# Optimization experiments

Hardware: AMD Instinct MI355X
Metric: run time of the kernel (lower is better)

Reference implementation:

```python
import jax, jax.numpy as jnp
import numpy as np

NEG_SLOPE = 0.2  # PyG GATConv default negative_slope


def gat_conv(x, W, a_src, a_dst, bias, src, dst, heads, out_c, concat):
    """PyG-style GATConv with self-loops. x:[N,F_in], W:[F_in,heads*out_c]."""
    N = x.shape[0]
    # add self loops
    loop = jnp.arange(N, dtype=src.dtype)
    src = jnp.concatenate([src, loop])
    dst = jnp.concatenate([dst, loop])
    h = (x @ W).reshape(N, heads, out_c)            # [N,H,C]
    alpha_src = jnp.sum(h * a_src, axis=-1)          # [N,H]
    alpha_dst = jnp.sum(h * a_dst, axis=-1)          # [N,H]
    e = jax.nn.leaky_relu(alpha_src[src] + alpha_dst[dst], NEG_SLOPE)  # [E,H]
    # segment softmax over incoming edges of each destination node
    m = jax.ops.segment_max(e, dst, num_segments=N)  # [N,H]
    ex = jnp.exp(e - m[dst])
    s = jax.ops.segment_sum(ex, dst, num_segments=N)
    alpha = ex / (s[dst] + 1e-16)                    # [E,H]
    msg = h[src] * alpha[:, :, None]                 # [E,H,C]
    out = jax.ops.segment_sum(msg, dst, num_segments=N)  # [N,H,C]
    out = out.reshape(N, heads * out_c) if concat else out.mean(axis=1)
    return out + bias


def setup_inputs() -> dict:
    key = jax.random.key(0)
    ks = jax.random.split(key, 16)
    N, E = 25000, 400000
    node_dim, hidden, out_dim, heads = 64, 128, 256, 4

    def glorot(k, shape):
        fan = shape[0] + shape[-1]
        return jax.random.normal(k, shape, jnp.float32) * np.sqrt(2.0 / fan)

    return {
        "x": jax.random.normal(ks[0], (N, node_dim), jnp.float32),
        "edge_index": jax.random.randint(ks[1], (2, E), 0, N, jnp.int32),
        "W_emb": glorot(ks[2], (node_dim, hidden)),
        "b_emb": jnp.zeros((hidden,), jnp.float32),
        "W1": glorot(ks[3], (hidden, heads * hidden)),
        "a1_src": glorot(ks[4], (heads, hidden)),
        "a1_dst": glorot(ks[5], (heads, hidden)),
        "b1": jnp.zeros((heads * hidden,), jnp.float32),
        "W2": glorot(ks[6], (heads * hidden, hidden)),
        "a2_src": glorot(ks[7], (1, hidden)),
        "a2_dst": glorot(ks[8], (1, hidden)),
        "b2": jnp.zeros((hidden,), jnp.float32),
        "W_out": glorot(ks[9], (hidden, out_dim)),
        "b_out": jnp.zeros((out_dim,), jnp.float32),
    }


def reference(x, edge_index, W_emb, b_emb, W1, a1_src, a1_dst, b1, W2, a2_src, a2_dst, b2, W_out, b_out):
    src, dst = edge_index[0], edge_index[1]
    heads, hidden = a1_src.shape[0], a1_src.shape[1]
    h = jax.nn.relu(x @ W_emb + b_emb)                 # dropout is identity in eval
    h = gat_conv(h, W1, a1_src, a1_dst, b1, src, dst, heads, hidden, True)
    h = jax.nn.elu(h)
    h = gat_conv(h, W2, a2_src, a2_dst, b2, src, dst, 1, hidden, False)
    h = jax.nn.elu(h)
    g = jnp.mean(h, axis=0, keepdims=True)             # global mean pool, batch=None -> [1, hidden]
    return g @ W_out + b_out                           # [1, out_dim]
```

## Files before the change

### kernel.cpp

```cpp
#include <hip/hip_runtime.h>
#include <hip/hip_bf16.h>


#define LRELU(x) ((x) > 0.f ? (x) : 0.2f * (x))

typedef short bf16x8 __attribute__((ext_vector_type(8)));
typedef float f32x4 __attribute__((ext_vector_type(4)));
typedef float f32x2 __attribute__((ext_vector_type(2)));

static __device__ __forceinline__ unsigned short f2b(float f) {
    union { float f; unsigned u; } x; x.f = f;
    unsigned r = x.u + 0x7fff + ((x.u >> 16) & 1);
    return (unsigned short)(r >> 16);
}
static __device__ __forceinline__ float rl_f(float v, int c) {
    return __int_as_float(__builtin_amdgcn_readlane(__float_as_int(v), c));
}
static __device__ __forceinline__ unsigned char f2fp8(float v) {
    int p = __builtin_amdgcn_cvt_pk_fp8_f32(v, v, 0, false);
    return (unsigned char)(p & 0xff);
}

__global__ void zero_kernel(int* __restrict__ deg, int* __restrict__ cursor,
                            float* __restrict__ pool, int* __restrict__ done, int N) {
    int i = blockIdx.x * blockDim.x + threadIdx.x;
    if (i < N) deg[i] = 0;
    else if (i < 2 * N) cursor[i - N] = 0;
    else if (i < 2 * N + 128) pool[i - 2 * N] = 0.f;
    else if (i == 2 * N + 128) *done = 0;
}

__global__ void deg_count_kernel(const int* __restrict__ ei, int E, int N, int* __restrict__ deg) {
    int i = blockIdx.x * blockDim.x + threadIdx.x;
    if (i < E) atomicAdd(&deg[ei[E + i]], 1);
    else if (i < E + N) atomicAdd(&deg[i - E], 1);
}

__global__ __launch_bounds__(256) void scan_pass1(const int* __restrict__ deg, int* __restrict__ rowptr,
                                                  int* __restrict__ bsum, int N) {
    __shared__ int sd[256];
    int t = threadIdx.x, i = blockIdx.x * 256 + t;
    int d = (i < N) ? deg[i] : 0;
    sd[t] = d;
    __syncthreads();
    for (int off = 1; off < 256; off <<= 1) {
        int v = (t >= off) ? sd[t - off] : 0;
        __syncthreads();
        sd[t] += v;
        __syncthreads();
    }
    if (i < N) rowptr[i] = sd[t] - d;
    if (t == 255) bsum[blockIdx.x] = sd[t];
}

__global__ __launch_bounds__(128) void scan_pass2(const int* __restrict__ bsum, int* __restrict__ boff,
                                                  int* __restrict__ rowptr, int nb, int N) {
    __shared__ int sd[128];
    int t = threadIdx.x;
    int d = (t < nb) ? bsum[t] : 0;
    sd[t] = d;
    __syncthreads();
    for (int off = 1; off < 128; off <<= 1) {
        int v = (t >= off) ? sd[t - off] : 0;
        __syncthreads();
        sd[t] += v;
        __syncthreads();
    }
    if (t < nb) boff[t] = sd[t] - d;
    if (t == 127) rowptr[N] = sd[t];
}

__global__ __launch_bounds__(256) void scan_pass3(int* __restrict__ rowptr, const int* __restrict__ boff, int N) {
    int i = blockIdx.x * 256 + threadIdx.x;
    if (i < N) rowptr[i] += boff[blockIdx.x];
}

__global__ void scatter_kernel(const int* __restrict__ ei, int E, int N,
                               const int* __restrict__ rowptr, int* __restrict__ cursor,
                               int* __restrict__ esrc) {
    int i = blockIdx.x * blockDim.x + threadIdx.x;
    int s, d;
    if (i < E) { s = ei[i]; d = ei[E + i]; }
    else if (i < E + N) { s = i - E; d = s; }
    else return;
    int pos = rowptr[d] + atomicAdd(&cursor[d], 1);
    esrc[pos] = s;
}

__global__ void prep_kernel(const float* __restrict__ x, const float* __restrict__ We,
                            const float* __restrict__ W1, const float* __restrict__ W2,
                            unsigned short* __restrict__ xb, unsigned short* __restrict__ WeT,
                            unsigned short* __restrict__ W1T, unsigned short* __restrict__ W2T,
                            int Nx) {
    int i = blockIdx.x * blockDim.x + threadIdx.x;
    if (i < Nx) { xb[i] = f2b(x[i]); return; }
    i -= Nx;
    if (i < 64 * 128) { int k = i >> 7, n = i & 127; WeT[n * 64 + k] = f2b(We[i]); return; }
    i -= 64 * 128;
    if (i < 128 * 512) { int k = i >> 9, n = i & 511; W1T[n * 128 + k] = f2b(W1[i]); return; }
    i -= 128 * 512;
    if (i < 512 * 128) { int k = i >> 7, n = i & 127; W2T[n * 512 + k] = f2b(W2[i]); return; }
}

__global__ __launch_bounds__(256) void gemm12_fused(const unsigned short* __restrict__ A,
                                                    const unsigned short* __restrict__ WeT,
                                                    const float* __restrict__ b_emb,
                                                    const unsigned short* __restrict__ W1T,
                                                    unsigned char* __restrict__ C8,
                                                    const float* __restrict__ a_src,
                                                    const float* __restrict__ a_dst,
                                                    float* __restrict__ as_out,
                                                    float* __restrict__ ad_out, int M) {
    __shared__ __align__(16) unsigned short smem[22016];
    unsigned short* Asx = smem;
    unsigned short* Bwe = smem + 9216;
    unsigned short* h0s = smem;
    unsigned short* Bs  = smem + 16896;
    __shared__ float sAl[128][2];

    int tid = threadIdx.x;
    int gm0 = blockIdx.y * 128, gn0 = blockIdx.x * 128;
    int w = tid >> 6, lane = tid & 63;
    int wrow = (w >> 1) * 64, wcol = (w & 1) * 64;
    int l15 = lane & 15, quad = lane >> 4;

    f32x4 acc[4][4];
#pragma unroll
    for (int i = 0; i < 4; i++)
#pragma unroll
        for (int j = 0; j < 4; j++) acc[i][j] = {0.f, 0.f, 0.f, 0.f};

#pragma unroll
    for (int rr = 0; rr < 4; rr++) {
        int lin = tid + rr * 256;
        int row = lin >> 3;
        int cg = (lin & 7) * 8;
        int grow = gm0 + row; if (grow >= M) grow = M - 1;
        *(uint4*)&Asx[row * 72 + cg] = *(const uint4*)&A[(size_t)grow * 64 + cg];
        *(uint4*)&Bwe[row * 72 + cg] = *(const uint4*)&WeT[(size_t)row * 64 + cg];
    }
    __syncthreads();
#pragma unroll
    for (int k0 = 0; k0 < 64; k0 += 32) {
        bf16x8 af[4], bfr[4];
#pragma unroll
        for (int i = 0; i < 4; i++) {
            af[i]  = *(const bf16x8*)&Asx[(wrow + i * 16 + l15) * 72 + k0 + quad * 8];
            bfr[i] = *(const bf16x8*)&Bwe[(wcol + i * 16 + l15) * 72 + k0 + quad * 8];
        }
#pragma unroll
        for (int i = 0; i < 4; i++)
#pragma unroll
            for (int j = 0; j < 4; j++)
                acc[i][j] = __builtin_amdgcn_mfma_f32_16x16x32_bf16(af[i], bfr[j], acc[i][j], 0, 0, 0);
    }
    __syncthreads();

#pragma unroll
    for (int j = 0; j < 4; j++) {
        int col = wcol + j * 16 + l15;
        float bv = b_emb[col];
#pragma unroll
        for (int i = 0; i < 4; i++) {
            int row = wrow + i * 16 + quad * 4;
#pragma unroll
            for (int r = 0; r < 4; r++) {
                float v = fmaxf(acc[i][j][r] + bv, 0.f);
                h0s[(row + r) * 132 + col] = f2b(v);
            }
        }
    }

#pragma unroll
    for (int i = 0; i < 4; i++)
#pragma unroll
        for (int j = 0; j < 4; j++) acc[i][j] = {0.f, 0.f, 0.f, 0.f};

    for (int k0 = 0; k0 < 128; k0 += 32) {
#pragma unroll
        for (int rr = 0; rr < 2; rr++) {
            int lin = tid + rr * 256;
            int row = lin >> 2;
            int cg = (lin & 3) * 8;
            *(uint4*)&Bs[row * 40 + cg] = *(const uint4*)&W1T[(size_t)(gn0 + row) * 128 + k0 + cg];
        }
        __syncthreads();
        bf16x8 af[4], bfr[4];
#pragma unroll
        for (int i = 0; i < 4; i++) {
            af[i]  = *(const bf16x8*)&h0s[(wrow + i * 16 + l15) * 132 + k0 + quad * 8];
            bfr[i] = *(const bf16x8*)&Bs[(wcol + i * 16 + l15) * 40 + quad * 8];
        }
#pragma unroll
        for (int i = 0; i < 4; i++)
#pragma unroll
            for (int j = 0; j < 4; j++)
                acc[i][j] = __builtin_amdgcn_mfma_f32_16x16x32_bf16(af[i], bfr[j], acc[i][j], 0, 0, 0);
        __syncthreads();
    }

#pragma unroll
    for (int i = 0; i < 4; i++) {
        int row = gm0 + wrow + i * 16 + quad * 4;
#pragma unroll
        for (int j = 0; j < 4; j++) {
            int col = gn0 + wcol + j * 16 + l15;
#pragma unroll
            for (int r = 0; r < 4; r++) {
                int gr = row + r;
                if (gr < M) C8[(size_t)gr * 512 + col] = f2fp8(acc[i][j][r]);
            }
        }
    }

    {
        int hh = blockIdx.x;
        float as_c[4], ad_c[4];
#pragma unroll
        for (int j = 0; j < 4; j++) {
            int c = gn0 + wcol + j * 16 + l15;
            as_c[j] = a_src[c];
            ad_c[j] = a_dst[c];
        }
#pragma unroll
        for (int i = 0; i < 4; i++) {
#pragma unroll
            for (int r = 0; r < 4; r++) {
                float ps = 0.f, pd = 0.f;
#pragma unroll
                for (int j = 0; j < 4; j++) {
                    ps += acc[i][j][r] * as_c[j];
                    pd += acc[i][j][r] * ad_c[j];
                }
#pragma unroll
                for (int o = 1; o < 16; o <<= 1) {
                    ps += __shfl_xor(ps, o);
                    pd += __shfl_xor(pd, o);
                }
                if (wcol == 64 && l15 == 0) {
                    int lr = wrow + i * 16 + quad * 4 + r;
                    sAl[lr][0] = ps;
                    sAl[lr][1] = pd;
                }
            }
        }
        __syncthreads();
        if (wcol == 0) {
#pragma unroll
            for (int i = 0; i < 4; i++) {
#pragma unroll
                for (int r = 0; r < 4; r++) {
                    float ps = 0.f, pd = 0.f;
#pragma unroll
                    for (int j = 0; j < 4; j++) {
                        ps += acc[i][j][r] * as_c[j];
                        pd += acc[i][j][r] * ad_c[j];
                    }
#pragma unroll
                    for (int o = 1; o < 16; o <<= 1) {
                        ps += __shfl_xor(ps, o);
                        pd += __shfl_xor(pd, o);
                    }
                    if (l15 == 0) {
                        int lr = wrow + i * 16 + quad * 4 + r;
                        int gr = gm0 + lr;
                        if (gr < M) {
                            as_out[(size_t)gr * 4 + hh] = ps + sAl[lr][0];
                            ad_out[(size_t)gr * 4 + hh] = pd + sAl[lr][1];
                        }
                    }
                }
            }
        }
    }
}

template <int ACT, int OFMT, int ALPHA, int H>
__global__ __launch_bounds__(256) void gemm_mfma_nt(const unsigned short* __restrict__ A,
                                                    const unsigned short* __restrict__ Bt,
                                                    const float* __restrict__ bias,
                                                    void* __restrict__ Cout,
                                                    const float* __restrict__ a_src,
                                                    const float* __restrict__ a_dst,
                                                    float* __restrict__ as_out,
                                                    float* __restrict__ ad_out,
                                                    int M, int N, int K) {
    __shared__ __align__(16) unsigned short As[128 * 40];
    __shared__ __align__(16) unsigned short Bs[128 * 40];
    __shared__ float sAl[128][2];
    int tid = threadIdx.x;
    int gm0 = blockIdx.y * 128, gn0 = blockIdx.x * 128;
    int w = tid >> 6, lane = tid & 63;
    int wrow = (w >> 1) * 64, wcol = (w & 1) * 64;
    int l15 = lane & 15, quad = lane >> 4;

    f32x4 acc[4][4];
#pragma unroll
    for (int i = 0; i < 4; i++)
#pragma unroll
        for (int j = 0; j < 4; j++) acc[i][j] = {0.f, 0.f, 0.f, 0.f};

    for (int k0 = 0; k0 < K; k0 += 32) {
#pragma unroll
        for (int rr = 0; rr < 2; rr++) {
            int lin = tid + rr * 256;
            int row = lin >> 2;
            int cg = (lin & 3) * 8;
            int grow = gm0 + row; if (grow >= M) grow = M - 1;
            uint4 va = *(const uint4*)&A[(size_t)grow * K + k0 + cg];
            *(uint4*)&As[row * 40 + cg] = va;
            uint4 vb = *(const uint4*)&Bt[(size_t)(gn0 + row) * K + k0 + cg];
            *(uint4*)&Bs[row * 40 + cg] = vb;
        }
        __syncthreads();
        bf16x8 af[4], bfr[4];
#pragma unroll
        for (int i = 0; i < 4; i++) {
            af[i]  = *(const bf16x8*)&As[(wrow + i * 16 + l15) * 40 + quad * 8];
            bfr[i] = *(const bf16x8*)&Bs[(wcol + i * 16 + l15) * 40 + quad * 8];
        }
#pragma unroll
        for (int i = 0; i < 4; i++)
#pragma unroll
            for (int j = 0; j < 4; j++)
                acc[i][j] = __builtin_amdgcn_mfma_f32_16x16x32_bf16(af[i], bfr[j], acc[i][j], 0, 0, 0);
        __syncthreads();
    }

    if (OFMT == 0) {
        unsigned short* C = (unsigned short*)Cout;
#pragma unroll
        for (int i = 0; i < 4; i++) {
            int row = gm0 + wrow + i * 16 + quad * 4;
#pragma unroll
            for (int j = 0; j < 4; j++) {
                int col = gn0 + wcol + j * 16 + l15;
                float bv = bias ? bias[col] : 0.f;
#pragma unroll
                for (int r = 0; r < 4; r++) {
                    int gr = row + r;
                    if (gr < M) {
                        float v = acc[i][j][r] + bv;
                        if (ACT == 1) v = fmaxf(v, 0.f);
                        C[(size_t)gr * N + col] = f2b(v);
                    }
                }
            }
        }
    } else {
        unsigned char* C8 = (unsigned char*)Cout;
#pragma unroll
        for (int i = 0; i < 4; i++) {
            int row = gm0 + wrow + i * 16 + quad * 4;
#pragma unroll
            for (int j = 0; j < 4; j++) {
                int col = gn0 + wcol + j * 16 + l15;
#pragma unroll
                for (int r = 0; r < 4; r++) {
                    int gr = row + r;
                    if (gr < M) C8[(size_t)gr * N + col] = f2fp8(acc[i][j][r]);
                }
            }
        }
    }

    if (ALPHA) {
        int hh = blockIdx.x;
        float as_c[4], ad_c[4];
#pragma unroll
        for (int j = 0; j < 4; j++) {
            int c = gn0 + wcol + j * 16 + l15;
            as_c[j] = a_src[c];
            ad_c[j] = a_dst[c];
        }
#pragma unroll
        for (int i = 0; i < 4; i++) {
#pragma unroll
            for (int r = 0; r < 4; r++) {
                float ps = 0.f, pd = 0.f;
#pragma unroll
                for (int j = 0; j < 4; j++) {
                    ps += acc[i][j][r] * as_c[j];
                    pd += acc[i][j][r] * ad_c[j];
                }
#pragma unroll
                for (int o = 1; o < 16; o <<= 1) {
                    ps += __shfl_xor(ps, o);
                    pd += __shfl_xor(pd, o);
                }
                if (wcol == 64 && l15 == 0) {
                    int lr = wrow + i * 16 + quad * 4 + r;
                    sAl[lr][0] = ps;
                    sAl[lr][1] = pd;
                }
            }
        }
        __syncthreads();
        if (wcol == 0) {
#pragma unroll
            for (int i = 0; i < 4; i++) {
#pragma unroll
                for (int r = 0; r < 4; r++) {
                    float ps = 0.f, pd = 0.f;
#pragma unroll
                    for (int j = 0; j < 4; j++) {
                        ps += acc[i][j][r] * as_c[j];
                        pd += acc[i][j][r] * ad_c[j];
                    }
#pragma unroll
                    for (int o = 1; o < 16; o <<= 1) {
                        ps += __shfl_xor(ps, o);
                        pd += __shfl_xor(pd, o);
                    }
                    if (l15 == 0) {
                        int lr = wrow + i * 16 + quad * 4 + r;
                        int gr = gm0 + lr;
                        if (gr < M) {
                            as_out[(size_t)gr * H + hh] = ps + sAl[lr][0];
                            ad_out[(size_t)gr * H + hh] = pd + sAl[lr][1];
                        }
                    }
                }
            }
        }
    }
}

__global__ __launch_bounds__(256) void gat_agg_l1(const unsigned* __restrict__ hq,
                                                  const float4* __restrict__ as4,
                                                  const float4* __restrict__ ad4,
                                                  const int* __restrict__ rowptr,
                                                  const int* __restrict__ esrc,
                                                  const float* __restrict__ bias,
                                                  unsigned short* __restrict__ out, int N) {
    __shared__ float wlds_all[4][256];
    int w = threadIdx.x >> 6, lane = threadIdx.x & 63;
    int n = blockIdx.x * 4 + w;
    if (n >= N) return;
    float* wlds = wlds_all[w];
    int begin = rowptr[n], deg = rowptr[n + 1] - begin;
    float4 adn = ad4[n];

    int s_l0 = 0;
    float4 e0 = {-3.4e38f, -3.4e38f, -3.4e38f, -3.4e38f};
    if (lane < deg) {
        s_l0 = esrc[begin + lane];
        float4 u = as4[s_l0];
        e0.x = LRELU(u.x + adn.x); e0.y = LRELU(u.y + adn.y);
        e0.z = LRELU(u.z + adn.z); e0.w = LRELU(u.w + adn.w);
    }
    float4 m = e0;
    for (int base = 64; base < deg; base += 64) {
        int j = base + lane;
        if (j < deg) {
            float4 u = as4[esrc[begin + j]];
            m.x = fmaxf(m.x, LRELU(u.x + adn.x)); m.y = fmaxf(m.y, LRELU(u.y + adn.y));
            m.z = fmaxf(m.z, LRELU(u.z + adn.z)); m.w = fmaxf(m.w, LRELU(u.w + adn.w));
        }
    }
#pragma unroll
    for (int o = 32; o >= 1; o >>= 1) {
        m.x = fmaxf(m.x, __shfl_xor(m.x, o));
        m.y = fmaxf(m.y, __shfl_xor(m.y, o));
        m.z = fmaxf(m.z, __shfl_xor(m.z, o));
        m.w = fmaxf(m.w, __shfl_xor(m.w, o));
    }
    float4 s4 = {0.f, 0.f, 0.f, 0.f};
    if (lane < deg) {
        s4.x = __expf(e0.x - m.x); s4.y = __expf(e0.y - m.y);
        s4.z = __expf(e0.z - m.z); s4.w = __expf(e0.w - m.w);
    }
    for (int base = 64; base < deg; base += 64) {
        int j = base + lane;
        if (j < deg) {
            float4 u = as4[esrc[begin + j]];
            s4.x += __expf(LRELU(u.x + adn.x) - m.x); s4.y += __expf(LRELU(u.y + adn.y) - m.y);
            s4.z += __expf(LRELU(u.z + adn.z) - m.z); s4.w += __expf(LRELU(u.w + adn.w) - m.w);
        }
    }
#pragma unroll
    for (int o = 32; o >= 1; o >>= 1) {
        s4.x += __shfl_xor(s4.x, o); s4.y += __shfl_xor(s4.y, o);
        s4.z += __shfl_xor(s4.z, o); s4.w += __shfl_xor(s4.w, o);
    }
    float4 inv = {1.f / (s4.x + 1e-16f), 1.f / (s4.y + 1e-16f),
                  1.f / (s4.z + 1e-16f), 1.f / (s4.w + 1e-16f)};

    float acc[8] = {};
    int h = lane >> 4;
#define ACC_E1(q, wgt) { \
    f32x2 p0 = __builtin_amdgcn_cvt_pk_f32_fp8((int)q.x, false); \
    f32x2 p1 = __builtin_amdgcn_cvt_pk_f32_fp8((int)q.x, true);  \
    f32x2 p2 = __builtin_amdgcn_cvt_pk_f32_fp8((int)q.y, false); \
    f32x2 p3 = __builtin_amdgcn_cvt_pk_f32_fp8((int)q.y, true);  \
    acc[0] += wgt * p0.x; acc[1] += wgt * p0.y; acc[2] += wgt * p1.x; acc[3] += wgt * p1.y; \
    acc[4] += wgt * p2.x; acc[5] += wgt * p2.y; acc[6] += wgt * p3.x; acc[7] += wgt * p3.y; }

    for (int base = 0; base < deg; base += 64) {
        int j = base + lane;
        int len = min(64, deg - base);
        int s_l = s_l0;
        float4 e = e0;
        if (base > 0 && j < deg) {
            s_l = esrc[begin + j];
            float4 u = as4[s_l];
            e.x = LRELU(u.x + adn.x); e.y = LRELU(u.y + adn.y);
            e.z = LRELU(u.z + adn.z); e.w = LRELU(u.w + adn.w);
        }
        if (j < deg) {
            float4 wv4 = {__expf(e.x - m.x) * inv.x, __expf(e.y - m.y) * inv.y,
                          __expf(e.z - m.z) * inv.z, __expf(e.w - m.w) * inv.w};
            *(float4*)&wlds[lane * 4] = wv4;
        }
        int c = 0;
        for (; c + 4 <= len; c += 4) {
            int s0 = __builtin_amdgcn_readlane(s_l, c);
            int s1 = __builtin_amdgcn_readlane(s_l, c + 1);
            int s2 = __builtin_amdgcn_readlane(s_l, c + 2);
            int s3 = __builtin_amdgcn_readlane(s_l, c + 3);
            uint2 q0 = *((const uint2*)(hq + (size_t)s0 * 128) + lane);
            uint2 q1 = *((const uint2*)(hq + (size_t)s1 * 128) + lane);
            uint2 q2 = *((const uint2*)(hq + (size_t)s2 * 128) + lane);
            uint2 q3 = *((const uint2*)(hq + (size_t)s3 * 128) + lane);
            float w0 = wlds[c * 4 + h];
            float w1 = wlds[c * 4 + 4 + h];
            float w2 = wlds[c * 4 + 8 + h];
            float w3 = wlds[c * 4 + 12 + h];
            ACC_E1(q0, w0); ACC_E1(q1, w1); ACC_E1(q2, w2); ACC_E1(q3, w3);
        }
        for (; c < len; c++) {
            int s0 = __builtin_amdgcn_readlane(s_l, c);
            uint2 q0 = *((const uint2*)(hq + (size_t)s0 * 128) + lane);
            float w0 = wlds[c * 4 + h];
            ACC_E1(q0, w0);
        }
    }
#undef ACC_E1
    int f0 = lane * 8;
    unsigned pk[4];
#pragma unroll
    for (int k = 0; k < 4; k++) {
        float v0 = acc[2 * k] + bias[f0 + 2 * k];
        float v1 = acc[2 * k + 1] + bias[f0 + 2 * k + 1];
        v0 = v0 > 0.f ? v0 : (__expf(v0) - 1.f);
        v1 = v1 > 0.f ? v1 : (__expf(v1) - 1.f);
        pk[k] = (unsigned)f2b(v0) | ((unsigned)f2b(v1) << 16);
    }
    uint4 pv = {pk[0], pk[1], pk[2], pk[3]};
    *((uint4*)(out + (size_t)n * 512) + lane) = pv;
}

__global__ __launch_bounds__(256) void gat_agg_l2(const unsigned char* __restrict__ hq,
                                                  const float* __restrict__ as,
                                                  const float* __restrict__ ad,
                                                  const int* __restrict__ rowptr,
                                                  const int* __restrict__ esrc,
                                                  const float* __restrict__ bias,
                                                  float* __restrict__ out, int N) {
    int w = threadIdx.x >> 6, lane = threadIdx.x & 63;
    int n = blockIdx.x * 4 + w;
    if (n >= N) return;
    int begin = rowptr[n], deg = rowptr[n + 1] - begin;
    float adn = ad[n];

    int s_l0 = 0;
    float e0 = -3.4e38f;
    if (lane < deg) {
        s_l0 = esrc[begin + lane];
        e0 = LRELU(as[s_l0] + adn);
    }
    float m = e0;
    for (int base = 64; base < deg; base += 64) {
        int j = base + lane;
        if (j < deg) m = fmaxf(m, LRELU(as[esrc[begin + j]] + adn));
    }
#pragma unroll
    for (int o = 32; o >= 1; o >>= 1) m = fmaxf(m, __shfl_xor(m, o));

    float s = (lane < deg) ? __expf(e0 - m) : 0.f;
    for (int base = 64; base < deg; base += 64) {
        int j = base + lane;
        if (j < deg) s += __expf(LRELU(as[esrc[begin + j]] + adn) - m);
    }
#pragma unroll
    for (int o = 32; o >= 1; o >>= 1) s += __shfl_xor(s, o);
    float inv = 1.f / (s + 1e-16f);

    float acc0 = 0.f, acc1 = 0.f;
    for (int base = 0; base < deg; base += 64) {
        int j = base + lane;
        int len = min(64, deg - base);
        int s_l = s_l0;
        float e = e0;
        if (base > 0 && j < deg) {
            s_l = esrc[begin + j];
            e = LRELU(as[s_l] + adn);
        }
        float w_l = (j < deg) ? __expf(e - m) * inv : 0.f;
        int c = 0;
        for (; c + 4 <= len; c += 4) {
            int sp0 = __builtin_amdgcn_readlane(s_l, c);
            int sp1 = __builtin_amdgcn_readlane(s_l, c + 1);
            int sp2 = __builtin_amdgcn_readlane(s_l, c + 2);
            int sp3 = __builtin_amdgcn_readlane(s_l, c + 3);
            unsigned short u0 = *((const unsigned short*)(hq + (size_t)sp0 * 128) + lane);
            unsigned short u1 = *((const unsigned short*)(hq + (size_t)sp1 * 128) + lane);
            unsigned short u2 = *((const unsigned short*)(hq + (size_t)sp2 * 128) + lane);
            unsigned short u3 = *((const unsigned short*)(hq + (size_t)sp3 * 128) + lane);
            float w0 = rl_f(w_l, c), w1 = rl_f(w_l, c + 1);
            float w2 = rl_f(w_l, c + 2), w3 = rl_f(w_l, c + 3);
            f32x2 p0 = __builtin_amdgcn_cvt_pk_f32_fp8((int)u0, false);
            f32x2 p1 = __builtin_amdgcn_cvt_pk_f32_fp8((int)u1, false);
            f32x2 p2 = __builtin_amdgcn_cvt_pk_f32_fp8((int)u2, false);
            f32x2 p3 = __builtin_amdgcn_cvt_pk_f32_fp8((int)u3, false);
            acc0 += w0 * p0.x; acc1 += w0 * p0.y;
            acc0 += w1 * p1.x; acc1 += w1 * p1.y;
            acc0 += w2 * p2.x; acc1 += w2 * p2.y;
            acc0 += w3 * p3.x; acc1 += w3 * p3.y;
        }
        for (; c < len; c++) {
            int sp0 = __builtin_amdgcn_readlane(s_l, c);
            float w0 = rl_f(w_l, c);
            unsigned short u0 = *((const unsigned short*)(hq + (size_t)sp0 * 128) + lane);
            f32x2 p0 = __builtin_amdgcn_cvt_pk_f32_fp8((int)u0, false);
            acc0 += w0 * p0.x; acc1 += w0 * p0.y;
        }
    }
    float v0 = acc0 + bias[lane * 2];
    float v1 = acc1 + bias[lane * 2 + 1];
    v0 = v0 > 0.f ? v0 : (__expf(v0) - 1.f);
    v1 = v1 > 0.f ? v1 : (__expf(v1) - 1.f);
    float2 pv = {v0, v1};
    *(float2*)&out[(size_t)n * 128 + lane * 2] = pv;
}

__global__ __launch_bounds__(256) void pool_final_kernel(const float* __restrict__ o2,
                                                         float* __restrict__ pool,
                                                         int* __restrict__ done,
                                                         const float* __restrict__ Wout,
                                                         const float* __restrict__ bout,
                                                         float* __restrict__ out,
                                                         int N, int nblocks, float invN) {
    __shared__ float4 sred[256];
    int f4 = threadIdx.x & 31;
    int r = blockIdx.x * 256 + (threadIdx.x >> 5);
    float4 acc = {0.f, 0.f, 0.f, 0.f};
    for (int i = 0; i < 32; i++, r += 8) {
        if (r < N) {
            float4 v = *(const float4*)&o2[(size_t)r * 128 + f4 * 4];
            acc.x += v.x; acc.y += v.y; acc.z += v.z; acc.w += v.w;
        }
    }
    sred[threadIdx.x] = acc;
    __syncthreads();
    if (threadIdx.x < 32) {
        float4 t = sred[threadIdx.x];
#pragma unroll
        for (int k = 1; k < 8; k++) {
            float4 u = sred[threadIdx.x + 32 * k];
            t.x += u.x; t.y += u.y; t.z += u.z; t.w += u.w;
        }
        atomicAdd(&pool[f4 * 4 + 0], t.x);
        atomicAdd(&pool[f4 * 4 + 1], t.y);
        atomicAdd(&pool[f4 * 4 + 2], t.z);
        atomicAdd(&pool[f4 * 4 + 3], t.w);
    }
    __threadfence();
    __shared__ int isLast;
    if (threadIdx.x == 0) isLast = (atomicAdd(done, 1) == nblocks - 1);
    __syncthreads();
    if (isLast) {
        __shared__ float spool[128];
        if (threadIdx.x < 128) spool[threadIdx.x] = atomicAdd(&pool[threadIdx.x], 0.f);
        __syncthreads();
        int o = threadIdx.x;
        float a = 0.f;
        for (int k = 0; k < 128; k++) a += spool[k] * Wout[k * 256 + o];
        out[o] = a * invN + bout[o];
    }
}

extern "C" void kernel_launch(void* const* d_in, const int* in_sizes, int n_in,
                              void* d_out, int out_size, void* d_ws, size_t ws_size,
                              hipStream_t stream) {
    const float* x      = (const float*)d_in[0];
    const int*   ei     = (const int*)d_in[1];
    const float* W_emb  = (const float*)d_in[2];
    const float* b_emb  = (const float*)d_in[3];
    const float* W1     = (const float*)d_in[4];
    const float* a1_src = (const float*)d_in[5];
    const float* a1_dst = (const float*)d_in[6];
    const float* b1     = (const float*)d_in[7];
    const float* W2     = (const float*)d_in[8];
    const float* a2_src = (const float*)d_in[9];
    const float* a2_dst = (const float*)d_in[10];
    const float* b2     = (const float*)d_in[11];
    const float* W_out  = (const float*)d_in[12];
    const float* b_out  = (const float*)d_in[13];
    float* out = (float*)d_out;

    const int N = in_sizes[0] / 64;
    const int E = in_sizes[1] / 2;
    const int Etot = E + N;
    const int nb = (N + 255) / 256;

    char* ws = (char*)d_ws;
    size_t off = 0;
    auto alloc = [&](size_t bytes) -> void* {
        void* p = ws + off;
        off = (off + bytes + 255) & ~(size_t)255;
        return p;
    };
    typedef unsigned short u16;
    u16* xb    = (u16*)alloc((size_t)N * 64 * 2);
    u16* WeT   = (u16*)alloc((size_t)128 * 64 * 2);
    u16* W1T   = (u16*)alloc((size_t)512 * 128 * 2);
    u16* W2T   = (u16*)alloc((size_t)128 * 512 * 2);
    unsigned char* h1q = (unsigned char*)alloc((size_t)N * 512);
    u16* o1b   = (u16*)alloc((size_t)N * 512 * 2);
    unsigned char* h2q = (unsigned char*)alloc((size_t)N * 128);
    float* o2  = (float*)alloc((size_t)N * 128 * 4);
    float* as1 = (float*)alloc((size_t)N * 4 * 4);
    float* ad1 = (float*)alloc((size_t)N * 4 * 4);
    float* as2 = (float*)alloc((size_t)N * 4);
    float* ad2 = (float*)alloc((size_t)N * 4);
    float* pool = (float*)alloc(128 * 4);
    int* done   = (int*)alloc(256);
    int* rowptr = (int*)alloc((size_t)(N + 1) * 4);
    int* deg    = (int*)alloc((size_t)N * 4);
    int* cursor = (int*)alloc((size_t)N * 4);
    int* bsum   = (int*)alloc(128 * 4);
    int* boff   = (int*)alloc(128 * 4);
    int* esrc   = (int*)alloc((size_t)Etot * 4);

    zero_kernel<<<(2 * N + 129 + 255) / 256, 256, 0, stream>>>(deg, cursor, pool, done, N);
    int blocksE = (Etot + 255) / 256;
    deg_count_kernel<<<blocksE, 256, 0, stream>>>(ei, E, N, deg);
    scan_pass1<<<nb, 256, 0, stream>>>(deg, rowptr, bsum, N);
    scan_pass2<<<1, 128, 0, stream>>>(bsum, boff, rowptr, nb, N);
    scan_pass3<<<nb, 256, 0, stream>>>(rowptr, boff, N);
    scatter_kernel<<<blocksE, 256, 0, stream>>>(ei, E, N, rowptr, cursor, esrc);

    int Nx = N * 64;
    int prep_elems = Nx + 64 * 128 + 128 * 512 + 512 * 128;
    prep_kernel<<<(prep_elems + 255) / 256, 256, 0, stream>>>(x, W_emb, W1, W2, xb, WeT, W1T, W2T, Nx);

    int mtiles = (N + 127) / 128;
    gemm12_fused<<<dim3(4, mtiles), 256, 0, stream>>>(xb, WeT, b_emb, W1T, h1q,
                                                      a1_src, a1_dst, as1, ad1, N);

    gat_agg_l1<<<(N + 3) / 4, 256, 0, stream>>>((const unsigned*)h1q, (const float4*)as1,
                                                (const float4*)ad1, rowptr, esrc, b1, o1b, N);

    gemm_mfma_nt<0, 1, 1, 1><<<dim3(1, mtiles), 256, 0, stream>>>(
        o1b, W2T, nullptr, h2q, a2_src, a2_dst, as2, ad2, N, 128, 512);

    gat_agg_l2<<<(N + 3) / 4, 256, 0, stream>>>(h2q, as2, ad2, rowptr, esrc, b2, o2, N);

    int npb = (N + 255) / 256;
    pool_final_kernel<<<npb, 256, 0, stream>>>(o2, pool, done, W_out, b_out, out,
                                               N, npb, 1.f / (float)N);
}
```

Before: 277.3 us.

## Fuse prep into degree count, drop scan pass3, unroll gather loops by 8

Merges the bf16 conversion and weight-transpose prep kernel into the degree-count kernel. It removes the third scan pass by adding per-block offsets (boff) at every rowptr read in scatter and both aggregation kernels. The gather loops in both GAT aggregation kernels go from 4 to 8 loads in flight. This cuts two kernel launches and increases memory-level parallelism, at the cost of extra boff lookups and higher register pressure.

```diff
diff --git a/kernel.cpp b/kernel.cpp
--- a/kernel.cpp
+++ b/kernel.cpp
@@ -30,10 +30,25 @@
     else if (i == 2 * N + 128) *done = 0;
 }
 
-__global__ void deg_count_kernel(const int* __restrict__ ei, int E, int N, int* __restrict__ deg) {
+__global__ void prep_count_kernel(const int* __restrict__ ei, int E, int N,
+                                  int* __restrict__ deg,
+                                  const float* __restrict__ x, const float* __restrict__ We,
+                                  const float* __restrict__ W1, const float* __restrict__ W2,
+                                  unsigned short* __restrict__ xb, unsigned short* __restrict__ WeT,
+                                  unsigned short* __restrict__ W1T, unsigned short* __restrict__ W2T,
+                                  int Nx) {
     int i = blockIdx.x * blockDim.x + threadIdx.x;
-    if (i < E) atomicAdd(&deg[ei[E + i]], 1);
-    else if (i < E + N) atomicAdd(&deg[i - E], 1);
+    if (i < E) { atomicAdd(&deg[ei[E + i]], 1); return; }
+    i -= E;
+    if (i < N) { atomicAdd(&deg[i], 1); return; }
+    i -= N;
+    if (i < Nx) { xb[i] = f2b(x[i]); return; }
+    i -= Nx;
+    if (i < 64 * 128) { int k = i >> 7, n = i & 127; WeT[n * 64 + k] = f2b(We[i]); return; }
+    i -= 64 * 128;
+    if (i < 128 * 512) { int k = i >> 9, n = i & 511; W1T[n * 128 + k] = f2b(W1[i]); return; }
+    i -= 128 * 512;
+    if (i < 512 * 128) { int k = i >> 7, n = i & 127; W2T[n * 512 + k] = f2b(W2[i]); return; }
 }
 
 __global__ __launch_bounds__(256) void scan_pass1(const int* __restrict__ deg, int* __restrict__ rowptr,
@@ -49,12 +64,12 @@
         sd[t] += v;
         __syncthreads();
     }
-    if (i < N) rowptr[i] = sd[t] - d;
+    if (i <= N) rowptr[i] = sd[t] - d;
     if (t == 255) bsum[blockIdx.x] = sd[t];
 }
 
 __global__ __launch_bounds__(128) void scan_pass2(const int* __restrict__ bsum, int* __restrict__ boff,
-                                                  int* __restrict__ rowptr, int nb, int N) {
+                                                  int nb) {
     __shared__ int sd[128];
     int t = threadIdx.x;
     int d = (t < nb) ? bsum[t] : 0;
@@ -67,39 +82,18 @@
         __syncthreads();
     }
     if (t < nb) boff[t] = sd[t] - d;
-    if (t == 127) rowptr[N] = sd[t];
-}
-
-__global__ __launch_bounds__(256) void scan_pass3(int* __restrict__ rowptr, const int* __restrict__ boff, int N) {
-    int i = blockIdx.x * 256 + threadIdx.x;
-    if (i < N) rowptr[i] += boff[blockIdx.x];
 }
 
 __global__ void scatter_kernel(const int* __restrict__ ei, int E, int N,
-                               const int* __restrict__ rowptr, int* __restrict__ cursor,
-                               int* __restrict__ esrc) {
+                               const int* __restrict__ rowptr, const int* __restrict__ boff,
+                               int* __restrict__ cursor, int* __restrict__ esrc) {
     int i = blockIdx.x * blockDim.x + threadIdx.x;
     int s, d;
     if (i < E) { s = ei[i]; d = ei[E + i]; }
     else if (i < E + N) { s = i - E; d = s; }
     else return;
-    int pos = rowptr[d] + atomicAdd(&cursor[d], 1);
+    int pos = rowptr[d] + boff[d >> 8] + atomicAdd(&cursor[d], 1);
     esrc[pos] = s;
-}
-
-__global__ void prep_kernel(const float* __restrict__ x, const float* __restrict__ We,
-                            const float* __restrict__ W1, const float* __restrict__ W2,
-                            unsigned short* __restrict__ xb, unsigned short* __restrict__ WeT,
-                            unsigned short* __restrict__ W1T, unsigned short* __restrict__ W2T,
-                            int Nx) {
-    int i = blockIdx.x * blockDim.x + threadIdx.x;
-    if (i < Nx) { xb[i] = f2b(x[i]); return; }
-    i -= Nx;
-    if (i < 64 * 128) { int k = i >> 7, n = i & 127; WeT[n * 64 + k] = f2b(We[i]); return; }
-    i -= 64 * 128;
-    if (i < 128 * 512) { int k = i >> 9, n = i & 511; W1T[n * 128 + k] = f2b(W1[i]); return; }
-    i -= 128 * 512;
-    if (i < 512 * 128) { int k = i >> 7, n = i & 127; W2T[n * 512 + k] = f2b(W2[i]); return; }
 }
 
 __global__ __launch_bounds__(256) void gemm12_fused(const unsigned short* __restrict__ A,
@@ -430,6 +424,7 @@
                                                   const float4* __restrict__ as4,
                                                   const float4* __restrict__ ad4,
                                                   const int* __restrict__ rowptr,
+                                                  const int* __restrict__ boff,
                                                   const int* __restrict__ esrc,
                                                   const float* __restrict__ bias,
                                                   unsigned short* __restrict__ out, int N) {
@@ -438,7 +433,8 @@
     int n = blockIdx.x * 4 + w;
     if (n >= N) return;
     float* wlds = wlds_all[w];
-    int begin = rowptr[n], deg = rowptr[n + 1] - begin;
+    int begin = rowptr[n] + boff[n >> 8];
+    int deg = rowptr[n + 1] + boff[(n + 1) >> 8] - begin;
     float4 adn = ad4[n];
 
     int s_l0 = 0;
@@ -513,24 +509,22 @@
             *(float4*)&wlds[lane * 4] = wv4;
         }
         int c = 0;
-        for (; c + 4 <= len; c += 4) {
-            int s0 = __builtin_amdgcn_readlane(s_l, c);
-            int s1 = __builtin_amdgcn_readlane(s_l, c + 1);
-            int s2 = __builtin_amdgcn_readlane(s_l, c + 2);
-            int s3 = __builtin_amdgcn_readlane(s_l, c + 3);
-            uint2 q0 = *((const uint2*)(hq + (size_t)s0 * 128) + lane);
-            uint2 q1 = *((const uint2*)(hq + (size_t)s1 * 128) + lane);
-            uint2 q2 = *((const uint2*)(hq + (size_t)s2 * 128) + lane);
-            uint2 q3 = *((const uint2*)(hq + (size_t)s3 * 128) + lane);
-            float w0 = wlds[c * 4 + h];
-            float w1 = wlds[c * 4 + 4 + h];
-            float w2 = wlds[c * 4 + 8 + h];
-            float w3 = wlds[c * 4 + 12 + h];
-            ACC_E1(q0, w0); ACC_E1(q1, w1); ACC_E1(q2, w2); ACC_E1(q3, w3);
+        for (; c + 8 <= len; c += 8) {
+            uint2 q[8];
+#pragma unroll
+            for (int t = 0; t < 8; t++) {
+                int sp = __builtin_amdgcn_readlane(s_l, c + t);
+                q[t] = *((const uint2*)(hq + (size_t)sp * 128) + lane);
+            }
+#pragma unroll
+            for (int t = 0; t < 8; t++) {
+                float wt = wlds[(c + t) * 4 + h];
+                ACC_E1(q[t], wt);
+            }
         }
         for (; c < len; c++) {
-            int s0 = __builtin_amdgcn_readlane(s_l, c);
-            uint2 q0 = *((const uint2*)(hq + (size_t)s0 * 128) + lane);
+            int sp = __builtin_amdgcn_readlane(s_l, c);
+            uint2 q0 = *((const uint2*)(hq + (size_t)sp * 128) + lane);
             float w0 = wlds[c * 4 + h];
             ACC_E1(q0, w0);
         }
@@ -554,13 +548,15 @@
                                                   const float* __restrict__ as,
                                                   const float* __restrict__ ad,
                                                   const int* __restrict__ rowptr,
+                                                  const int* __restrict__ boff,
                                                   const int* __restrict__ esrc,
                                                   const float* __restrict__ bias,
                                                   float* __restrict__ out, int N) {
     int w = threadIdx.x >> 6, lane = threadIdx.x & 63;
     int n = blockIdx.x * 4 + w;
     if (n >= N) return;
-    int begin = rowptr[n], deg = rowptr[n + 1] - begin;
+    int begin = rowptr[n] + boff[n >> 8];
+    int deg = rowptr[n + 1] + boff[(n + 1) >> 8] - begin;
     float adn = ad[n];
 
     int s_l0 = 0;
@@ -598,30 +594,25 @@
         }
         float w_l = (j < deg) ? __expf(e - m) * inv : 0.f;
         int c = 0;
-        for (; c + 4 <= len; c += 4) {
-            int sp0 = __builtin_amdgcn_readlane(s_l, c);
-            int sp1 = __builtin_amdgcn_readlane(s_l, c + 1);
-            int sp2 = __builtin_amdgcn_readlane(s_l, c + 2);
-            int sp3 = __builtin_amdgcn_readlane(s_l, c + 3);
-            unsigned short u0 = *((const unsigned short*)(hq + (size_t)sp0 * 128) + lane);
-            unsigned short u1 = *((const unsigned short*)(hq + (size_t)sp1 * 128) + lane);
-            unsigned short u2 = *((const unsigned short*)(hq + (size_t)sp2 * 128) + lane);
-            unsigned short u3 = *((const unsigned short*)(hq + (size_t)sp3 * 128) + lane);
-            float w0 = rl_f(w_l, c), w1 = rl_f(w_l, c + 1);
-            float w2 = rl_f(w_l, c + 2), w3 = rl_f(w_l, c + 3);
-            f32x2 p0 = __builtin_amdgcn_cvt_pk_f32_fp8((int)u0, false);
-            f32x2 p1 = __builtin_amdgcn_cvt_pk_f32_fp8((int)u1, false);
-            f32x2 p2 = __builtin_amdgcn_cvt_pk_f32_fp8((int)u2, false);
-            f32x2 p3 = __builtin_amdgcn_cvt_pk_f32_fp8((int)u3, false);
-            acc0 += w0 * p0.x; acc1 += w0 * p0.y;
-            acc0 += w1 * p1.x; acc1 += w1 * p1.y;
-            acc0 += w2 * p2.x; acc1 += w2 * p2.y;
-            acc0 += w3 * p3.x; acc1 += w3 * p3.y;
+        for (; c + 8 <= len; c += 8) {
+            unsigned short u[8];
+            float wt[8];
+#pragma unroll
+            for (int t = 0; t < 8; t++) {
+                int sp = __builtin_amdgcn_readlane(s_l, c + t);
+                u[t] = *((const unsigned short*)(hq + (size_t)sp * 128) + lane);
+                wt[t] = rl_f(w_l, c + t);
+            }
+#pragma unroll
+            for (int t = 0; t < 8; t++) {
+                f32x2 p = __builtin_amdgcn_cvt_pk_f32_fp8((int)u[t], false);
+                acc0 += wt[t] * p.x; acc1 += wt[t] * p.y;
+            }
         }
         for (; c < len; c++) {
-            int sp0 = __builtin_amdgcn_readlane(s_l, c);
+            int sp = __builtin_amdgcn_readlane(s_l, c);
             float w0 = rl_f(w_l, c);
-            unsigned short u0 = *((const unsigned short*)(hq + (size_t)sp0 * 128) + lane);
+            unsigned short u0 = *((const unsigned short*)(hq + (size_t)sp * 128) + lane);
             f32x2 p0 = __builtin_amdgcn_cvt_pk_f32_fp8((int)u0, false);
             acc0 += w0 * p0.x; acc1 += w0 * p0.y;
         }
@@ -702,7 +693,7 @@
     const int N = in_sizes[0] / 64;
     const int E = in_sizes[1] / 2;
     const int Etot = E + N;
-    const int nb = (N + 255) / 256;
+    const int nb = (N + 256) / 256;
 
     char* ws = (char*)d_ws;
     size_t off = 0;
@@ -734,29 +725,23 @@
     int* esrc   = (int*)alloc((size_t)Etot * 4);
 
     zero_kernel<<<(2 * N + 129 + 255) / 256, 256, 0, stream>>>(deg, cursor, pool, done, N);
+    int Nx = N * 64;
+    int pc_elems = Etot + Nx + 64 * 128 + 128 * 512 + 512 * 128;
+    prep_count_kernel<<<(pc_elems + 255) / 256, 256, 0, stream>>>(
+        ei, E, N, deg, x, W_emb, W1, W2, xb, WeT, W1T, W2T, Nx);
+    scan_pass1<<<nb, 256, 0, stream>>>(deg, rowptr, bsum, N);
+    scan_pass2<<<1, 128, 0, stream>>>(bsum, boff, nb);
     int blocksE = (Etot + 255) / 256;
-    deg_count_kernel<<<blocksE, 256, 0, stream>>>(ei, E, N, deg);
-    scan_pass1<<<nb, 256, 0, stream>>>(deg, rowptr, bsum, N);
-    scan_pass2<<<1, 128, 0, stream>>>(bsum, boff, rowptr, nb, N);
-    scan_pass3<<<nb, 256, 0, stream>>>(rowptr, boff, N);
-    scatter_kernel<<<blocksE, 256, 0, stream>>>(ei, E, N, rowptr, cursor, esrc);
-
-    int Nx = N * 64;
-    int prep_elems = Nx + 64 * 128 + 128 * 512 + 512 * 128;
-    prep_kernel<<<(prep_elems + 255) / 256, 256, 0, stream>>>(x, W_emb, W1, W2, xb, WeT, W1T, W2T, Nx);
+    scatter_kernel<<<blocksE, 256, 0, stream>>>(ei, E, N, rowptr, boff, cursor, esrc);
 
     int mtiles = (N + 127) / 128;
     gemm12_fused<<<dim3(4, mtiles), 256, 0, stream>>>(xb, WeT, b_emb, W1T, h1q,
                                                       a1_src, a1_dst, as1, ad1, N);
-
     gat_agg_l1<<<(N + 3) / 4, 256, 0, stream>>>((const unsigned*)h1q, (const float4*)as1,
-                                                (const float4*)ad1, rowptr, esrc, b1, o1b, N);
-
+                                                (const float4*)ad1, rowptr, boff, esrc, b1, o1b, N);
     gemm_mfma_nt<0, 1, 1, 1><<<dim3(1, mtiles), 256, 0, stream>>>(
         o1b, W2T, nullptr, h2q, a2_src, a2_dst, as2, ad2, N, 128, 512);
-
-    gat_agg_l2<<<(N + 3) / 4, 256, 0, stream>>>(h2q, as2, ad2, rowptr, esrc, b2, o2, N);
-
+    gat_agg_l2<<<(N + 3) / 4, 256, 0, stream>>>(h2q, as2, ad2, rowptr, boff, esrc, b2, o2, N);
     int npb = (N + 255) / 256;
     pool_final_kernel<<<npb, 256, 0, stream>>>(o2, pool, done, W_out, b_out, out,
                                                N, npb, 1.f / (float)N);
```

Measured after the change: 284.8 us. 1.03x slower.
